# Optimization experiments

Hardware: AMD Instinct MI355X
Metric: run time of the kernel (lower is better)

Reference implementation:

```python
import jax, jax.numpy as jnp
import numpy as np

M = 150        # AR2 tail-fit window
LAM = 1e-3     # ridge regularizer in the 2x2 solve
CLIP_K = 4.0   # soft clip multiplier
H = 96         # forecast horizon (base_model.H)


def setup_inputs() -> dict:
    key = jax.random.key(0)
    k1, k2 = jax.random.split(key)
    x = jax.random.normal(k1, (32, 512, 2048), dtype=jnp.float32)
    W = jax.random.normal(k2, (2048, 96), dtype=jnp.float32) * 0.02
    return {"x": x, "W": W}


def _ar2_forecast(x):
    # x: (B, C, L); closed-form AR2 fit on last M samples, vectorized over (B, C)
    y = x[..., -M:]                     # (B, C, M)
    Y = y[..., 2:]                      # targets
    p1 = y[..., 1:-1]
    p2 = y[..., :-2]
    s = lambda a, b: jnp.sum(a * b, axis=-1)
    A11 = s(p1, p1) + LAM
    A22 = s(p2, p2) + LAM
    A12 = s(p1, p2)
    b1 = s(p1, Y)
    b2 = s(p2, Y)
    det = A11 * A22 - A12 * A12
    a1 = (b1 * A22 - b2 * A12) / det    # (B, C)
    a2 = (A11 * b2 - A12 * b1) / det

    def step(carry, _):
        y1, y2 = carry
        yn = a1 * y1 + a2 * y2
        return (yn, y1), yn

    _, out = jax.lax.scan(step, (x[..., -1], x[..., -2]), None, length=H)
    return jnp.moveaxis(out, 0, -1)     # (B, C, H)


def reference(x, W):
    # AR2 part is computed on detached history in the original (numpy round-trip)
    Yb = jax.lax.stop_gradient(_ar2_forecast(x))
    d_hat = jnp.einsum('bcl,lh->bch', x, W)          # base model: per-channel linear head
    y_hat = Yb + d_hat
    last = x[..., -1:]                               # (B, C, 1), broadcasts over H
    hstd = jnp.maximum(jnp.std(x, axis=-1, ddof=1, keepdims=True), 1e-6)  # torch unbiased std
    return jnp.clip(y_hat, last - CLIP_K * hstd, last + CLIP_K * hstd)
```

## Files before the change

kernel.cpp:

```cpp
#include <hip/hip_runtime.h>
#include <math.h>

constexpr int L     = 2048;
constexpr int NH    = 96;
constexpr int MLEN  = 150;
constexpr int NAR   = 148;
constexpr float LAM    = 0.001f;
constexpr float CLIP_K = 4.0f;

constexpr int TM    = 32;
constexpr int STEPS = L / 32;

typedef __attribute__((ext_vector_type(8))) short short8;
typedef __attribute__((ext_vector_type(4))) float floatx4;

__device__ inline short f2bf(float f) {
    union { float f; unsigned u; } v; v.f = f;
    unsigned r = v.u + 0x7FFFu + ((v.u >> 16) & 1u);
    return (short)(r >> 16);
}

__global__ __launch_bounds__(256) void wt_kernel(
    const float* __restrict__ W, short* __restrict__ Wt)
{
    int idx = blockIdx.x * 256 + threadIdx.x;
    int n = idx >> 11;
    int k = idx & 2047;
    Wt[idx] = f2bf(W[k * NH + n]);
}

__global__ __launch_bounds__(256) void gemm_ar2_kernel(
    const float* __restrict__ x, const short* __restrict__ Wt,
    float* __restrict__ out)
{
    __shared__ float As[2][TM * 32];
    __shared__ float Ys[TM][NH + 1];
    __shared__ float los[TM], his[TM];

    const int t    = threadIdx.x;
    const int lane = t & 63;
    const int wv   = t >> 6;
    const int h    = wv >> 1;
    const int g    = wv & 1;
    const int m    = lane & 15;
    const int quad = lane >> 4;
    const int row0 = blockIdx.x * TM;
    const int r    = h * 16 + m;

    const int sr = wv * 8 + (lane >> 3);
    const int sc = lane & 7;
    const int gc = sc ^ (sr & 7);
    const float* sgptr = x + (size_t)(row0 + sr) * L + gc * 4;

    const short* wbase = Wt + (size_t)(48 * g + m) * L + quad * 8;

    floatx4 acc[3];
    #pragma unroll
    for (int jj = 0; jj < 3; ++jj) acc[jj] = floatx4{0.f, 0.f, 0.f, 0.f};

    float sum = 0.f, sumsq = 0.f;

    __builtin_amdgcn_global_load_lds(
        (const __attribute__((address_space(1))) unsigned int*)sgptr,
        (__attribute__((address_space(3))) unsigned int*)&As[0][wv * 256],
        16, 0, 0);
    short8 b_c[3], b_n[3];
    #pragma unroll
    for (int jj = 0; jj < 3; ++jj)
        b_c[jj] = *(const short8*)(wbase + jj * 16 * L);

    const int p0 = (2 * quad)     ^ (r & 7);
    const int p1 = (2 * quad + 1) ^ (r & 7);

    for (int s = 0; s < STEPS; ++s) {
        const int cur = s & 1;
        __syncthreads();

        if (s + 1 < STEPS)
            __builtin_amdgcn_global_load_lds(
                (const __attribute__((address_space(1))) unsigned int*)(sgptr + (s + 1) * 32),
                (__attribute__((address_space(3))) unsigned int*)&As[cur ^ 1][wv * 256],
                16, 0, 0);

        const int k1 = (s + 1 < STEPS) ? (s + 1) * 32 : s * 32;
        #pragma unroll
        for (int jj = 0; jj < 3; ++jj)
            b_n[jj] = *(const short8*)(wbase + jj * 16 * L + k1);

        float4 f0 = *(const float4*)(&As[cur][r * 32 + p0 * 4]);
        float4 f1 = *(const float4*)(&As[cur][r * 32 + p1 * 4]);

        if (g == 0) {
            sum  += ((f0.x + f0.y) + (f0.z + f0.w))
                  + ((f1.x + f1.y) + (f1.z + f1.w));
            sumsq = fmaf(f0.x, f0.x, sumsq); sumsq = fmaf(f0.y, f0.y, sumsq);
            sumsq = fmaf(f0.z, f0.z, sumsq); sumsq = fmaf(f0.w, f0.w, sumsq);
            sumsq = fmaf(f1.x, f1.x, sumsq); sumsq = fmaf(f1.y, f1.y, sumsq);
            sumsq = fmaf(f1.z, f1.z, sumsq); sumsq = fmaf(f1.w, f1.w, sumsq);
        }

        short8 af;
        af[0] = f2bf(f0.x); af[1] = f2bf(f0.y); af[2] = f2bf(f0.z); af[3] = f2bf(f0.w);
        af[4] = f2bf(f1.x); af[5] = f2bf(f1.y); af[6] = f2bf(f1.z); af[7] = f2bf(f1.w);

        #pragma unroll
        for (int jj = 0; jj < 3; ++jj)
            acc[jj] = __builtin_amdgcn_mfma_f32_16x16x32_bf16(af, b_c[jj], acc[jj], 0, 0, 0);

        #pragma unroll
        for (int jj = 0; jj < 3; ++jj) b_c[jj] = b_n[jj];
    }

    if (g == 0) {
        sum   += __shfl_xor(sum,   16); sum   += __shfl_xor(sum,   32);
        sumsq += __shfl_xor(sumsq, 16); sumsq += __shfl_xor(sumsq, 32);

        const float* ytail = x + (size_t)(row0 + r) * L + (L - MLEN);
        float A11 = 0.f, A22 = 0.f, A12 = 0.f, b1 = 0.f, b2 = 0.f;
        for (int i = quad; i < NAR; i += 4) {
            float p2v = ytail[i];
            float p1v = ytail[i + 1];
            float Yv  = ytail[i + 2];
            A11 = fmaf(p1v, p1v, A11);
            A22 = fmaf(p2v, p2v, A22);
            A12 = fmaf(p1v, p2v, A12);
            b1  = fmaf(p1v, Yv,  b1);
            b2  = fmaf(p2v, Yv,  b2);
        }
        A11 += __shfl_xor(A11, 16); A11 += __shfl_xor(A11, 32);
        A22 += __shfl_xor(A22, 16); A22 += __shfl_xor(A22, 32);
        A12 += __shfl_xor(A12, 16); A12 += __shfl_xor(A12, 32);
        b1  += __shfl_xor(b1,  16); b1  += __shfl_xor(b1,  32);
        b2  += __shfl_xor(b2,  16); b2  += __shfl_xor(b2,  32);

        if (quad == 0) {
            A11 += LAM; A22 += LAM;
            float det = A11 * A22 - A12 * A12;
            float a1c = (b1 * A22 - b2 * A12) / det;
            float a2c = (A11 * b2 - A12 * b1) / det;

            float last = ytail[MLEN - 1];
            float y1 = last;
            float y2 = ytail[MLEN - 2];
            for (int n = 0; n < NH; ++n) {
                float yn = a1c * y1 + a2c * y2;
                Ys[r][n] = yn;
                y2 = y1; y1 = yn;
            }
            float var  = (sumsq - sum * sum * (1.0f / L)) * (1.0f / (L - 1));
            float hstd = fmaxf(sqrtf(fmaxf(var, 0.f)), 1e-6f);
            los[r] = last - CLIP_K * hstd;
            his[r] = last + CLIP_K * hstd;
        }
    }
    __syncthreads();

    #pragma unroll
    for (int reg = 0; reg < 4; ++reg) {
        int rl = h * 16 + quad * 4 + reg;
        float lo = los[rl], hi = his[rl];
        #pragma unroll
        for (int jj = 0; jj < 3; ++jj) {
            int c = (3 * g + jj) * 16 + m;
            float v = acc[jj][reg] + Ys[rl][c];
            v = fminf(fmaxf(v, lo), hi);
            out[(size_t)(row0 + rl) * NH + c] = v;
        }
    }
}

extern "C" void kernel_launch(void* const* d_in, const int* in_sizes, int n_in,
                              void* d_out, int out_size, void* d_ws, size_t ws_size,
                              hipStream_t stream) {
    const float* x = (const float*)d_in[0];
    const float* W = (const float*)d_in[1];
    float* out = (float*)d_out;
    short* Wt  = (short*)d_ws;

    wt_kernel<<<dim3((NH * L) / 256), dim3(256), 0, stream>>>(W, Wt);

    const int rows = 32 * 512;
    gemm_ar2_kernel<<<dim3(rows / TM), dim3(256), 0, stream>>>(x, Wt, out);
}
```

Baseline: 234.9 us.

## Stage W tiles through LDS and double K-step to 64 per sync

Loads the bf16 weight tile for each K-slice into shared memory with asynchronous global-to-LDS copies, alongside the x tile, instead of each wave reading its B fragments straight from global memory into registers. It also doubles the K chunk per barrier from 32 to 64, halving the number of syncs. The goal is to cut redundant global and L2 traffic for W and reduce barrier overhead. In exchange it uses more LDS per block, which may lower occupancy, and adds extra LDS reads on the compute path.

```diff
diff --git a/kernel.cpp b/kernel.cpp
--- a/kernel.cpp
+++ b/kernel.cpp
@@ -8,8 +8,9 @@
 constexpr float LAM    = 0.001f;
 constexpr float CLIP_K = 4.0f;
 
-constexpr int TM    = 32;
-constexpr int STEPS = L / 32;
+constexpr int TM     = 32;
+constexpr int KM     = 64;
+constexpr int MSTEPS = L / KM;
 
 typedef __attribute__((ext_vector_type(8))) short short8;
 typedef __attribute__((ext_vector_type(4))) float floatx4;
@@ -33,7 +34,8 @@
     const float* __restrict__ x, const short* __restrict__ Wt,
     float* __restrict__ out)
 {
-    __shared__ float As[2][TM * 32];
+    __shared__ float As[2][TM * KM];
+    __shared__ short Bs[2][NH * KM];
     __shared__ float Ys[TM][NH + 1];
     __shared__ float los[TM], his[TM];
 
@@ -47,68 +49,77 @@
     const int row0 = blockIdx.x * TM;
     const int r    = h * 16 + m;
 
-    const int sr = wv * 8 + (lane >> 3);
-    const int sc = lane & 7;
-    const int gc = sc ^ (sr & 7);
-    const float* sgptr = x + (size_t)(row0 + sr) * L + gc * 4;
+    const int cA0 = wv * 128 + lane, cA1 = cA0 + 64;
+    const int rA0 = cA0 >> 4, chA0 = cA0 & 15;
+    const int rA1 = cA1 >> 4, chA1 = cA1 & 15;
+    const float* pa0 = x + (size_t)(row0 + rA0) * L
+                         + ((chA0 >> 3) * 32 + ((chA0 & 7) ^ (rA0 & 7)) * 4);
+    const float* pa1 = x + (size_t)(row0 + rA1) * L
+                         + ((chA1 >> 3) * 32 + ((chA1 & 7) ^ (rA1 & 7)) * 4);
 
-    const short* wbase = Wt + (size_t)(48 * g + m) * L + quad * 8;
+    const int cB0 = wv * 192 + lane, cB1 = cB0 + 64, cB2 = cB0 + 128;
+    const short* pb0 = Wt + (size_t)(cB0 >> 3) * L + (((cB0 & 7) ^ ((cB0 >> 3) & 7)) * 8);
+    const short* pb1 = Wt + (size_t)(cB1 >> 3) * L + (((cB1 & 7) ^ ((cB1 >> 3) & 7)) * 8);
+    const short* pb2 = Wt + (size_t)(cB2 >> 3) * L + (((cB2 & 7) ^ ((cB2 >> 3) & 7)) * 8);
 
     floatx4 acc[3];
     #pragma unroll
     for (int jj = 0; jj < 3; ++jj) acc[jj] = floatx4{0.f, 0.f, 0.f, 0.f};
-
     float sum = 0.f, sumsq = 0.f;
 
-    __builtin_amdgcn_global_load_lds(
-        (const __attribute__((address_space(1))) unsigned int*)sgptr,
-        (__attribute__((address_space(3))) unsigned int*)&As[0][wv * 256],
-        16, 0, 0);
-    short8 b_c[3], b_n[3];
-    #pragma unroll
-    for (int jj = 0; jj < 3; ++jj)
-        b_c[jj] = *(const short8*)(wbase + jj * 16 * L);
+    const int pA0 = (2 * quad)     ^ (m & 7);
+    const int pA1 = (2 * quad + 1) ^ (m & 7);
 
-    const int p0 = (2 * quad)     ^ (r & 7);
-    const int p1 = (2 * quad + 1) ^ (r & 7);
+    auto stage = [&](int buf, int k0) {
+        __builtin_amdgcn_global_load_lds(
+            (const __attribute__((address_space(1))) unsigned int*)(pa0 + k0),
+            (__attribute__((address_space(3))) unsigned int*)&As[buf][wv * 512], 16, 0, 0);
+        __builtin_amdgcn_global_load_lds(
+            (const __attribute__((address_space(1))) unsigned int*)(pa1 + k0),
+            (__attribute__((address_space(3))) unsigned int*)&As[buf][wv * 512 + 256], 16, 0, 0);
+        __builtin_amdgcn_global_load_lds(
+            (const __attribute__((address_space(1))) unsigned int*)(pb0 + k0),
+            (__attribute__((address_space(3))) unsigned int*)&Bs[buf][wv * 1536], 16, 0, 0);
+        __builtin_amdgcn_global_load_lds(
+            (const __attribute__((address_space(1))) unsigned int*)(pb1 + k0),
+            (__attribute__((address_space(3))) unsigned int*)&Bs[buf][wv * 1536 + 512], 16, 0, 0);
+        __builtin_amdgcn_global_load_lds(
+            (const __attribute__((address_space(1))) unsigned int*)(pb2 + k0),
+            (__attribute__((address_space(3))) unsigned int*)&Bs[buf][wv * 1536 + 1024], 16, 0, 0);
+    };
 
-    for (int s = 0; s < STEPS; ++s) {
+    stage(0, 0);
+
+    for (int s = 0; s < MSTEPS; ++s) {
         const int cur = s & 1;
         __syncthreads();
-
-        if (s + 1 < STEPS)
-            __builtin_amdgcn_global_load_lds(
-                (const __attribute__((address_space(1))) unsigned int*)(sgptr + (s + 1) * 32),
-                (__attribute__((address_space(3))) unsigned int*)&As[cur ^ 1][wv * 256],
-                16, 0, 0);
-
-        const int k1 = (s + 1 < STEPS) ? (s + 1) * 32 : s * 32;
-        #pragma unroll
-        for (int jj = 0; jj < 3; ++jj)
-            b_n[jj] = *(const short8*)(wbase + jj * 16 * L + k1);
-
-        float4 f0 = *(const float4*)(&As[cur][r * 32 + p0 * 4]);
-        float4 f1 = *(const float4*)(&As[cur][r * 32 + p1 * 4]);
-
-        if (g == 0) {
-            sum  += ((f0.x + f0.y) + (f0.z + f0.w))
-                  + ((f1.x + f1.y) + (f1.z + f1.w));
-            sumsq = fmaf(f0.x, f0.x, sumsq); sumsq = fmaf(f0.y, f0.y, sumsq);
-            sumsq = fmaf(f0.z, f0.z, sumsq); sumsq = fmaf(f0.w, f0.w, sumsq);
-            sumsq = fmaf(f1.x, f1.x, sumsq); sumsq = fmaf(f1.y, f1.y, sumsq);
-            sumsq = fmaf(f1.z, f1.z, sumsq); sumsq = fmaf(f1.w, f1.w, sumsq);
-        }
-
-        short8 af;
-        af[0] = f2bf(f0.x); af[1] = f2bf(f0.y); af[2] = f2bf(f0.z); af[3] = f2bf(f0.w);
-        af[4] = f2bf(f1.x); af[5] = f2bf(f1.y); af[6] = f2bf(f1.z); af[7] = f2bf(f1.w);
+        if (s + 1 < MSTEPS) stage(cur ^ 1, (s + 1) * KM);
 
         #pragma unroll
-        for (int jj = 0; jj < 3; ++jj)
-            acc[jj] = __builtin_amdgcn_mfma_f32_16x16x32_bf16(af, b_c[jj], acc[jj], 0, 0, 0);
+        for (int ss = 0; ss < 2; ++ss) {
+            float4 f0 = *(const float4*)&As[cur][r * KM + ss * 32 + pA0 * 4];
+            float4 f1 = *(const float4*)&As[cur][r * KM + ss * 32 + pA1 * 4];
 
-        #pragma unroll
-        for (int jj = 0; jj < 3; ++jj) b_c[jj] = b_n[jj];
+            if (g == 0) {
+                sum  += ((f0.x + f0.y) + (f0.z + f0.w))
+                      + ((f1.x + f1.y) + (f1.z + f1.w));
+                sumsq = fmaf(f0.x, f0.x, sumsq); sumsq = fmaf(f0.y, f0.y, sumsq);
+                sumsq = fmaf(f0.z, f0.z, sumsq); sumsq = fmaf(f0.w, f0.w, sumsq);
+                sumsq = fmaf(f1.x, f1.x, sumsq); sumsq = fmaf(f1.y, f1.y, sumsq);
+                sumsq = fmaf(f1.z, f1.z, sumsq); sumsq = fmaf(f1.w, f1.w, sumsq);
+            }
+
+            short8 af;
+            af[0] = f2bf(f0.x); af[1] = f2bf(f0.y); af[2] = f2bf(f0.z); af[3] = f2bf(f0.w);
+            af[4] = f2bf(f1.x); af[5] = f2bf(f1.y); af[6] = f2bf(f1.z); af[7] = f2bf(f1.w);
+
+            const int bch = ((ss * 4 + quad) ^ (m & 7)) * 8;
+            #pragma unroll
+            for (int jj = 0; jj < 3; ++jj) {
+                short8 bf = *(const short8*)&Bs[cur][(g * 48 + jj * 16 + m) * KM + bch];
+                acc[jj] = __builtin_amdgcn_mfma_f32_16x16x32_bf16(af, bf, acc[jj], 0, 0, 0);
+            }
+        }
     }
 
     if (g == 0) {
```

Result: faster. 205.9 us (-12.4%).
